# Kernel tuning notes

Measured on AMD Instinct MI355X. Metric: run time of the kernel, lower is better.

Reference implementation:

```python
import jax, jax.numpy as jnp
import numpy as np

N_NODES = 50000
N_EDGES = 800000
N_REL = 8
DIM = 256


def setup_inputs() -> dict:
    key = jax.random.key(0)
    ks = jax.random.split(key, 6)
    x = jax.random.normal(ks[0], (N_NODES, DIM), dtype=jnp.float32)
    # xavier-uniform-ish scale for [R, in, out] weights
    limit = float(np.sqrt(6.0 / (DIM + DIM)))
    W0 = jax.random.uniform(ks[1], (N_REL, DIM, DIM), dtype=jnp.float32, minval=-limit, maxval=limit)
    W1 = jax.random.uniform(ks[2], (N_REL, DIM, DIM), dtype=jnp.float32, minval=-limit, maxval=limit)
    b0 = jnp.zeros((DIM,), dtype=jnp.float32)
    b1 = jnp.zeros((DIM,), dtype=jnp.float32)
    edge_index = jax.random.randint(ks[3], (2, N_EDGES), 0, N_NODES, dtype=jnp.int64)
    edge_type = jax.random.randint(ks[4], (N_EDGES,), 0, N_REL, dtype=jnp.int64)
    return {"x": x, "W0": W0, "b0": b0, "W1": W1, "b1": b1,
            "edge_index": edge_index, "edge_type": edge_type}


def _rgcn_layer(x, W, b, src, dst, edge_type, num_nodes):
    # grouped GEMM over all relations: [R, N, out]
    xt = jnp.einsum('ni,rio->rno', x, W)
    # per-edge message = relu(x[src] @ W[edge_type] + b)  -> [E, out]
    msg = jax.nn.relu(xt[edge_type, src] + b)
    # scatter-add into destination nodes
    return jax.ops.segment_sum(msg, dst, num_segments=num_nodes)


def reference(x, W0, b0, W1, b1, edge_index, edge_type):
    src, dst = edge_index[0], edge_index[1]
    h = _rgcn_layer(x, W0, b0, src, dst, edge_type, x.shape[0])
    h = _rgcn_layer(h, W1, b1, src, dst, edge_type, x.shape[0])
    return h
```

## Files before the change

kernel.cpp:

```cpp
#include <hip/hip_runtime.h>

#define DIM 256
#define N_REL 8
#define NBLK 256
#define NBH 256

typedef __attribute__((ext_vector_type(8))) short short8_t;
typedef __attribute__((ext_vector_type(4))) float float4_t;

__device__ inline unsigned short f2bf(float f) {
    unsigned u = __float_as_uint(f);
    u += 0x7FFFu + ((u >> 16) & 1u);
    return (unsigned short)(u >> 16);
}
__device__ inline float bf2f(unsigned short h) {
    return __uint_as_float(((unsigned)h) << 16);
}

__global__ __launch_bounds__(256) void prep_mega(
    const float* __restrict__ x, unsigned short* __restrict__ xb, int n4,
    const float* __restrict__ W0, unsigned short* __restrict__ Wt0,
    const float* __restrict__ W1, unsigned short* __restrict__ Wt1,
    int nCast, int nW)
{
    __shared__ float tile[32][33];
    const int b = blockIdx.x;
    const int t = threadIdx.x;
    if (b < nCast) {
        const int i = b * 256 + t;
        if (i < n4) {
            const float4 v = ((const float4*)x)[i];
            ushort4 o;
            o.x = f2bf(v.x); o.y = f2bf(v.y); o.z = f2bf(v.z); o.w = f2bf(v.w);
            ((ushort4*)xb)[i] = o;
        }
    } else {
        const int wi = b - nCast;
        const float* W = (wi < nW) ? W0 : W1;
        unsigned short* Wt = (wi < nW) ? Wt0 : Wt1;
        const int bb = (wi < nW) ? wi : wi - nW;
        const int rel = bb >> 6;
        const int bx = bb & 7, by = (bb >> 3) & 7;
        const int i0 = bx * 32, o0 = by * 32;
        const int tx = t & 31, ty = t >> 5;
        const float* Wr = W + (size_t)rel * DIM * DIM;
        unsigned short* Wtr = Wt + (size_t)rel * DIM * DIM;
#pragma unroll
        for (int j = 0; j < 4; j++)
            tile[ty + 8 * j][tx] = Wr[(size_t)(i0 + ty + 8 * j) * DIM + o0 + tx];
        __syncthreads();
#pragma unroll
        for (int j = 0; j < 4; j++)
            Wtr[(size_t)(o0 + ty + 8 * j) * DIM + i0 + tx] =
                f2bf(tile[tx][ty + 8 * j]);
    }
}

__global__ __launch_bounds__(256) void build_keys_hist(
    const int* __restrict__ src, const int* __restrict__ dst,
    const int* __restrict__ et, int E,
    unsigned long long* __restrict__ e0, int* __restrict__ hist)
{
    __shared__ int lh[NBH];
    const int t = threadIdx.x, b = blockIdx.x;
    lh[t] = 0;
    __syncthreads();
    const int chunk = (E + NBLK - 1) / NBLK;
    const int lo = b * chunk, hi = min(lo + chunk, E);
    for (int i = lo + t; i < hi; i += 256) {
        const unsigned d = (unsigned)dst[i];
        e0[i] = ((unsigned long long)d << 32) |
                ((unsigned)((et[i] << 16) | src[i]));
        atomicAdd(&lh[d >> 8], 1);
    }
    __syncthreads();
    hist[t * NBLK + b] = lh[t];
}

__global__ __launch_bounds__(256) void scan_g_blocksums(
    const int* __restrict__ a, int n, int* __restrict__ bsum)
{
    __shared__ int red[256];
    const int t = threadIdx.x;
    const int base = blockIdx.x * 1024 + t * 4;
    int s = 0;
#pragma unroll
    for (int j = 0; j < 4; j++) {
        const int i = base + j;
        if (i < n) s += a[i];
    }
    red[t] = s;
    __syncthreads();
#pragma unroll
    for (int off = 128; off > 0; off >>= 1) {
        if (t < off) red[t] += red[t + off];
        __syncthreads();
    }
    if (t == 0) bsum[blockIdx.x] = red[0];
}

__global__ __launch_bounds__(256) void scan_g_write(
    const int* __restrict__ a, int n, const int* __restrict__ bsum, int nb,
    int* __restrict__ outArr, int* __restrict__ totalSlot)
{
    __shared__ int sb[64];
    __shared__ int sh[256];
    const int t = threadIdx.x;
    if (t < 64) sb[t] = (t < nb) ? bsum[t] : 0;
    __syncthreads();
    for (int off = 1; off < 64; off <<= 1) {
        int v = 0;
        if (t < 64) v = sb[t] + ((t >= off) ? sb[t - off] : 0);
        __syncthreads();
        if (t < 64) sb[t] = v;
        __syncthreads();
    }
    const int run0 = (blockIdx.x == 0) ? 0 : sb[blockIdx.x - 1];
    const int total = sb[nb - 1];

    const int base = blockIdx.x * 1024 + t * 4;
    int v[4];
#pragma unroll
    for (int j = 0; j < 4; j++) {
        const int i = base + j;
        v[j] = (i < n) ? a[i] : 0;
    }
    sh[t] = v[0] + v[1] + v[2] + v[3];
    __syncthreads();
    for (int off = 1; off < 256; off <<= 1) {
        const int add = (t >= off) ? sh[t - off] : 0;
        __syncthreads();
        sh[t] += add;
        __syncthreads();
    }
    int run = run0 + ((t == 0) ? 0 : sh[t - 1]);
#pragma unroll
    for (int j = 0; j < 4; j++) {
        const int i = base + j;
        if (i < n) outArr[i] = run;
        run += v[j];
    }
    if (totalSlot && (int)blockIdx.x == nb - 1 && t == 255) *totalSlot = total;
}

__global__ __launch_bounds__(256) void scatter_pass1(
    const unsigned long long* __restrict__ e0, int E,
    const int* __restrict__ histx, unsigned long long* __restrict__ e1)
{
    __shared__ int lbase[NBH];
    __shared__ int lrun[NBH];
    const int t = threadIdx.x, b = blockIdx.x;
    lbase[t] = histx[t * NBLK + b];
    lrun[t] = 0;
    __syncthreads();
    const int chunk = (E + NBLK - 1) / NBLK;
    const int lo = b * chunk, hi = min(lo + chunk, E);
    for (int i = lo + t; i < hi; i += 256) {
        const unsigned long long v = e0[i];
        const int bin = (int)(v >> 40) & 0xFF;
        const int pos = lbase[bin] + atomicAdd(&lrun[bin], 1);
        e1[pos] = v;
    }
}

__global__ __launch_bounds__(256) void bucket_sort(
    const unsigned long long* __restrict__ e1, int E,
    const int* __restrict__ histx,
    unsigned* __restrict__ ep, int* __restrict__ cnt)
{
    __shared__ int lh[256], lincl[256], lexcl[256], lrun[256];
    const int t = threadIdx.x;
    const int h = blockIdx.x;
    const int start = histx[h * NBLK];
    const int end = (h == NBH - 1) ? E : histx[(h + 1) * NBLK];
    if (end <= start) return;
    lh[t] = 0;
    __syncthreads();
    for (int i = start + t; i < end; i += 256)
        atomicAdd(&lh[(int)(e1[i] >> 32) & 0xFF], 1);
    __syncthreads();
    const int v = lh[t];
    lincl[t] = v;
    __syncthreads();
    for (int off = 1; off < 256; off <<= 1) {
        const int add = (t >= off) ? lincl[t - off] : 0;
        __syncthreads();
        lincl[t] += add;
        __syncthreads();
    }
    lexcl[t] = lincl[t] - v;
    lrun[t] = 0;
    if (v > 0) cnt[(h << 8) | t] = v;
    __syncthreads();
    for (int i = start + t; i < end; i += 256) {
        const unsigned long long x = e1[i];
        const int low = (int)(x >> 32) & 0xFF;
        const int pos = lexcl[low] + atomicAdd(&lrun[low], 1);
        ep[start + pos] = (unsigned)(x & 0xFFFFFFFFu);
    }
}

__global__ __launch_bounds__(256) void gemm_mfma_bias_relu(
    const unsigned short* __restrict__ Xb,
    const unsigned short* __restrict__ Wtb,
    const float* __restrict__ bias,
    unsigned short* __restrict__ Yall, int M, int Rtiles)
{
    __shared__ __align__(16) short smem[16384];

    const unsigned L = blockIdx.x;
    const int xcd = L & 7;
    const unsigned g = L >> 3;
    const int combo = g & 15;
    const int rt = (int)((g >> 4) << 3) | xcd;
    if (rt >= Rtiles) return;
    const int m0 = rt * 128;
    const int n0 = (combo & 1) * 128;
    const int rel = combo >> 1;

    const unsigned short* Wt = Wtb + (size_t)rel * DIM * DIM;
    unsigned short* Y = Yall + (size_t)rel * M * DIM;

    const int t = threadIdx.x;
    const int lane = t & 63;
    const int w = t >> 6;
    const int wr = w & 1, wc = w >> 1;
    const int r = lane & 15, q = lane >> 4;

    const int sl = lane & 3;
    const int rsub = lane >> 2;
    const unsigned short* gA[2];
    const unsigned short* gB[2];
#pragma unroll
    for (int h = 0; h < 2; h++) {
        const int row = h * 64 + w * 16 + rsub;
        const int gseg = sl ^ ((row >> 1) & 3);
        gA[h] = Xb + (size_t)(m0 + row) * DIM + gseg * 8;
        gB[h] = Wt + (size_t)(n0 + row) * DIM + gseg * 8;
    }

    const int swz = (q ^ ((r >> 1) & 3)) * 8;
    int offA[4], offB[4];
#pragma unroll
    for (int mi = 0; mi < 4; mi++)
        offA[mi] = (wr * 64 + mi * 16 + r) * 32 + swz;
#pragma unroll
    for (int ni = 0; ni < 4; ni++)
        offB[ni] = (wc * 64 + ni * 16 + r) * 32 + swz;

    float4_t acc[4][4];
#pragma unroll
    for (int i = 0; i < 4; i++)
#pragma unroll
        for (int j = 0; j < 4; j++) {
            float4_t z = {0.f, 0.f, 0.f, 0.f};
            acc[i][j] = z;
        }

#define STAGE(ks, bsel)                                                         \
    {                                                                           \
        const int k0_ = (ks) * 32;                                              \
        short* Ad_ = smem + ((bsel) ? 8192 : 0);                                \
        short* Bd_ = Ad_ + 4096;                                                \
        _Pragma("unroll")                                                       \
        for (int h = 0; h < 2; h++) {                                           \
            __builtin_amdgcn_global_load_lds(                                   \
                (const __attribute__((address_space(1))) unsigned int*)(gA[h] + k0_), \
                (__attribute__((address_space(3))) unsigned int*)(Ad_ + h * 2048 + w * 512), \
                16, 0, 0);                                                      \
            __builtin_amdgcn_global_load_lds(                                   \
                (const __attribute__((address_space(1))) unsigned int*)(gB[h] + k0_), \
                (__attribute__((address_space(3))) unsigned int*)(Bd_ + h * 2048 + w * 512), \
                16, 0, 0);                                                      \
        }                                                                       \
    }

    STAGE(0, 0);
#pragma unroll 1
    for (int ks = 0; ks < 8; ks++) {
        const int cur = ks & 1;
        if (ks < 7) {
            STAGE(ks + 1, cur ^ 1);
            asm volatile("s_waitcnt vmcnt(4)" ::: "memory");
        } else {
            asm volatile("s_waitcnt vmcnt(0)" ::: "memory");
        }
        asm volatile("s_barrier" ::: "memory");

        const short* As_b = smem + (cur ? 8192 : 0);
        const short* Bs_b = As_b + 4096;
        short8_t af[4], bf[4];
#pragma unroll
        for (int mi = 0; mi < 4; mi++)
            af[mi] = *(const short8_t*)&As_b[offA[mi]];
#pragma unroll
        for (int ni = 0; ni < 4; ni++)
            bf[ni] = *(const short8_t*)&Bs_b[offB[ni]];
#pragma unroll
        for (int mi = 0; mi < 4; mi++)
#pragma unroll
            for (int ni = 0; ni < 4; ni++)
                acc[mi][ni] = __builtin_amdgcn_mfma_f32_16x16x32_bf16(
                    af[mi], bf[ni], acc[mi][ni], 0, 0, 0);
        asm volatile("s_barrier" ::: "memory");
    }
#undef STAGE

    short* St = smem;

    float bv[4];
#pragma unroll
    for (int ni = 0; ni < 4; ni++)
        bv[ni] = bias[n0 + wc * 64 + ni * 16 + r];

#pragma unroll
    for (int mp = 0; mp < 2; mp++) {
#pragma unroll
        for (int s = 0; s < 2; s++) {
#pragma unroll
            for (int ni = 0; ni < 4; ni++) {
#pragma unroll
                for (int e = 0; e < 4; e++) {
                    const int rl = s * 32 + wr * 16 + q * 4 + e;
                    const int col = wc * 64 + ni * 16 + r;
                    St[rl * 136 + col] =
                        f2bf(fmaxf(acc[mp * 2 + s][ni][e] + bv[ni], 0.f));
                }
            }
        }
        __syncthreads();
#pragma unroll
        for (int j = 0; j < 4; j++) {
            const int id = t + 256 * j;
            const int rl2 = id >> 4;
            const int ch = id & 15;
            const int s = rl2 >> 5;
            const int rl = rl2 & 31;
            const int grow = m0 + (rl >> 4) * 64 + (mp * 2 + s) * 16 + (rl & 15);
            const short8_t v = *(const short8_t*)&St[rl2 * 136 + ch * 8];
            if (grow < M)
                *(short8_t*)&Y[(size_t)grow * DIM + n0 + ch * 8] = v;
        }
        if (mp == 0) __syncthreads();
    }
}

template <typename OT>
__global__ __launch_bounds__(256) void aggregate2x(
    const unsigned short* __restrict__ yall,
    const unsigned* __restrict__ ep, const int* __restrict__ rowptr,
    OT* __restrict__ out, int M)
{
    const int lane = threadIdx.x & 63;
    const int half = lane >> 5;
    const int cl = lane & 31;
    const int wv = (blockIdx.x * blockDim.x + threadIdx.x) >> 6;
    const int nw = (gridDim.x * blockDim.x) >> 6;
    const size_t plane = (size_t)M * DIM;
    const int npair = (M + 1) >> 1;

    for (int pr = wv; pr < npair; pr += nw) {
        const int d = 2 * pr + half;
        const bool live = (d < M);
        double acc[8];
#pragma unroll
        for (int j = 0; j < 8; j++) acc[j] = 0.0;

        int beg = 0, end = 0;
        if (live) { beg = rowptr[d]; end = rowptr[d + 1]; }

        for (int c0 = beg; c0 < end; c0 += 32) {
            const int n = min(32, end - c0);
            const unsigned myep = (c0 + cl < end) ? ep[c0 + cl] : 0u;
            for (int i = 0; i < n; i += 4) {
                short8_t u[4];
#pragma unroll
                for (int j = 0; j < 4; j++) {
                    const unsigned p = __shfl(myep, half * 32 + ((i + j) & 31));
                    u[j] = *(const short8_t*)(
                        yall + (size_t)(p >> 16) * plane +
                        (size_t)(p & 0xFFFFu) * DIM + cl * 8);
                }
#pragma unroll
                for (int j = 0; j < 4; j++) {
                    if (i + j < n) {
#pragma unroll
                        for (int k = 0; k < 8; k++)
                            acc[k] += (double)bf2f((unsigned short)u[j][k]);
                    }
                }
            }
        }
        if (live) {
            OT* dp = out + (size_t)d * DIM + cl * 8;
            if (sizeof(OT) == 4) {
                *(float4*)((float*)dp) = make_float4(
                    (float)acc[0], (float)acc[1], (float)acc[2], (float)acc[3]);
                *(float4*)((float*)dp + 4) = make_float4(
                    (float)acc[4], (float)acc[5], (float)acc[6], (float)acc[7]);
            } else {
                short8_t v;
#pragma unroll
                for (int j = 0; j < 8; j++) v[j] = (short)f2bf((float)acc[j]);
                *(short8_t*)((unsigned short*)dp) = v;
            }
        }
    }
}

__global__ __launch_bounds__(256) void gemm_bias_relu_f32(
    const float* __restrict__ A, const float* __restrict__ B,
    const float* __restrict__ bias, float* __restrict__ Y, int M)
{
    __shared__ float Asf[16][132];
    __shared__ float Bsf[16][128];
    const int t = threadIdx.x;
    const int tx = t & 15, ty = t >> 4;
    const int row0 = blockIdx.x * 128, col0 = blockIdx.y * 128;
    float acc[8][8];
#pragma unroll
    for (int i = 0; i < 8; i++)
#pragma unroll
        for (int j = 0; j < 8; j++) acc[i][j] = 0.f;
    const int arow = t >> 2, akseg = (t & 3) * 4;
    const int bk0 = t >> 5, bcol = (t & 31) * 4;
    for (int k0 = 0; k0 < DIM; k0 += 16) {
#pragma unroll
        for (int h = 0; h < 2; h++) {
            const int row = row0 + arow + h * 64;
            float4 av = (row < M) ? *(const float4*)(A + (size_t)row * DIM + k0 + akseg)
                                  : make_float4(0, 0, 0, 0);
            Asf[akseg + 0][arow + h * 64] = av.x;
            Asf[akseg + 1][arow + h * 64] = av.y;
            Asf[akseg + 2][arow + h * 64] = av.z;
            Asf[akseg + 3][arow + h * 64] = av.w;
        }
#pragma unroll
        for (int h = 0; h < 2; h++) {
            const int krow = bk0 + h * 8;
            *(float4*)&Bsf[krow][bcol] =
                *(const float4*)(B + (size_t)(k0 + krow) * DIM + col0 + bcol);
        }
        __syncthreads();
#pragma unroll
        for (int k = 0; k < 16; k++) {
            float a[8], b[8];
            *(float4*)&a[0] = *(const float4*)&Asf[k][ty * 4];
            *(float4*)&a[4] = *(const float4*)&Asf[k][64 + ty * 4];
            *(float4*)&b[0] = *(const float4*)&Bsf[k][tx * 4];
            *(float4*)&b[4] = *(const float4*)&Bsf[k][64 + tx * 4];
#pragma unroll
            for (int i = 0; i < 8; i++)
#pragma unroll
                for (int j = 0; j < 8; j++) acc[i][j] = fmaf(a[i], b[j], acc[i][j]);
        }
        __syncthreads();
    }
#pragma unroll
    for (int im = 0; im < 2; im++)
#pragma unroll
        for (int i = 0; i < 4; i++) {
            const int row = row0 + im * 64 + ty * 4 + i;
            if (row >= M) continue;
#pragma unroll
            for (int jm = 0; jm < 2; jm++) {
                const int col = col0 + jm * 64 + tx * 4;
                const float4 bb = *(const float4*)(bias + col);
                float4 o;
                o.x = fmaxf(acc[im * 4 + i][jm * 4 + 0] + bb.x, 0.f);
                o.y = fmaxf(acc[im * 4 + i][jm * 4 + 1] + bb.y, 0.f);
                o.z = fmaxf(acc[im * 4 + i][jm * 4 + 2] + bb.z, 0.f);
                o.w = fmaxf(acc[im * 4 + i][jm * 4 + 3] + bb.w, 0.f);
                *(float4*)(Y + (size_t)row * DIM + col) = o;
            }
        }
}

__global__ __launch_bounds__(256) void scatter_rel(
    const float* __restrict__ y, const int* __restrict__ src,
    const int* __restrict__ dst, const int* __restrict__ et,
    int rel, float* __restrict__ out, int n_edges)
{
    const int lane = threadIdx.x & 63;
    const int wave = (blockIdx.x * blockDim.x + threadIdx.x) >> 6;
    const int nwaves = (gridDim.x * blockDim.x) >> 6;
    for (int e = wave; e < n_edges; e += nwaves) {
        if (et[e] != rel) continue;
        const float4 v = *(const float4*)(y + (size_t)src[e] * DIM + lane * 4);
        float* o = out + (size_t)dst[e] * DIM + lane * 4;
        atomicAdd(o + 0, v.x);
        atomicAdd(o + 1, v.y);
        atomicAdd(o + 2, v.z);
        atomicAdd(o + 3, v.w);
    }
}

static inline size_t align16(size_t x) { return (x + 15) & ~(size_t)15; }

extern "C" void kernel_launch(void* const* d_in, const int* in_sizes, int n_in,
                              void* d_out, int out_size, void* d_ws, size_t ws_size,
                              hipStream_t stream)
{
    const float* x  = (const float*)d_in[0];
    const float* W0 = (const float*)d_in[1];
    const float* b0 = (const float*)d_in[2];
    const float* W1 = (const float*)d_in[3];
    const float* b1 = (const float*)d_in[4];
    const int* eidx = (const int*)d_in[5];
    const int* etyp = (const int*)d_in[6];

    const int M = in_sizes[0] / DIM;
    const int E = in_sizes[6];
    const int* src = eidx;
    const int* dst = eidx + E;
    float* out = (float*)d_out;

    const size_t plane = (size_t)M * DIM;
    const size_t wbytes = (size_t)N_REL * DIM * DIM * 2;
    const size_t yall_bytes = (size_t)N_REL * plane * 2;

    const size_t need = align16(plane * 2)
                      + align16(plane * 2)
                      + 2 * align16(wbytes)
                      + align16((size_t)(M + 1) * 4)
                      + align16((size_t)M * 4)
                      + align16((size_t)256 * 4)
                      + align16((size_t)NBH * NBLK * 4)
                      + align16((size_t)E * 4)
                      + align16(yall_bytes);

    if (M < 65536 && ws_size >= need && yall_bytes >= 2 * (size_t)E * 8) {
        char* ws = (char*)d_ws;
        size_t off = 0;
        unsigned short* h1b  = (unsigned short*)(ws + off); off = align16(off + plane * 2);
        unsigned short* xb   = (unsigned short*)(ws + off); off = align16(off + plane * 2);
        unsigned short* Wt0b = (unsigned short*)(ws + off); off = align16(off + wbytes);
        unsigned short* Wt1b = (unsigned short*)(ws + off); off = align16(off + wbytes);
        int* rowptr = (int*)(ws + off); off = align16(off + (size_t)(M + 1) * 4);
        int* cnt    = (int*)(ws + off); off = align16(off + (size_t)M * 4);
        int* bsum   = (int*)(ws + off); off = align16(off + (size_t)256 * 4);
        int* hist   = (int*)(ws + off); off = align16(off + (size_t)NBH * NBLK * 4);
        unsigned* ep = (unsigned*)(ws + off); off = align16(off + (size_t)E * 4);
        unsigned short* yall = (unsigned short*)(ws + off);
        unsigned long long* e64a = (unsigned long long*)yall;
        unsigned long long* e64b = e64a + E;

        const int n4 = (int)(plane / 4);
        const int nCast = (n4 + 255) / 256;
        const int nW = 512;
        prep_mega<<<nCast + 2 * nW, 256, 0, stream>>>(
            x, xb, n4, W0, Wt0b, W1, Wt1b, nCast, nW);

        hipMemsetAsync(cnt, 0, (size_t)M * 4, stream);
        build_keys_hist<<<NBLK, 256, 0, stream>>>(src, dst, etyp, E, e64a, hist);
        const int nhist = NBH * NBLK;
        const int nbh = (nhist + 1023) / 1024;
        scan_g_blocksums<<<nbh, 256, 0, stream>>>(hist, nhist, bsum);
        scan_g_write<<<nbh, 256, 0, stream>>>(hist, nhist, bsum, nbh, hist, (int*)nullptr);
        scatter_pass1<<<NBLK, 256, 0, stream>>>(e64a, E, hist, e64b);
        bucket_sort<<<NBH, 256, 0, stream>>>(e64b, E, hist, ep, cnt);
        const int nb = (M + 1023) / 1024;
        scan_g_blocksums<<<nb, 256, 0, stream>>>(cnt, M, bsum);
        scan_g_write<<<nb, 256, 0, stream>>>(cnt, M, bsum, nb, rowptr, &rowptr[M]);

        const int Rtiles = (M + 127) / 128;
        const int octets = (Rtiles + 7) / 8;
        const int ggrid = octets * 16 * 8;
        const int npair = (M + 1) / 2;
        const int agrid = (npair * 64 + 255) / 256;

        gemm_mfma_bias_relu<<<ggrid, 256, 0, stream>>>(xb, Wt0b, b0, yall, M, Rtiles);
        aggregate2x<unsigned short><<<agrid, 256, 0, stream>>>(yall, ep, rowptr, h1b, M);
        gemm_mfma_bias_relu<<<ggrid, 256, 0, stream>>>(h1b, Wt1b, b1, yall, M, Rtiles);
        aggregate2x<float><<<agrid, 256, 0, stream>>>(yall, ep, rowptr, out, M);
    } else {
        float* h1 = (float*)d_ws;
        float* y  = (float*)d_ws + plane;
        const dim3 gblk(256), ggrid2((M + 127) / 128, DIM / 128);
        hipMemsetAsync(h1, 0, plane * 4, stream);
        for (int r = 0; r < N_REL; r++) {
            gemm_bias_relu_f32<<<ggrid2, gblk, 0, stream>>>(
                x, W0 + (size_t)r * DIM * DIM, b0, y, M);
            scatter_rel<<<1024, 256, 0, stream>>>(y, src, dst, etyp, r, h1, E);
        }
        hipMemsetAsync(out, 0, plane * 4, stream);
        for (int r = 0; r < N_REL; r++) {
            gemm_bias_relu_f32<<<ggrid2, gblk, 0, stream>>>(
                h1, W1 + (size_t)r * DIM * DIM, b1, y, M);
            scatter_rel<<<1024, 256, 0, stream>>>(y, src, dst, etyp, r, out, E);
        }
    }
}
```

Before: 469.3 us.

## Split relations into two groups of four to halve the per-relation GEMM output buffer

Edges are now sorted by relation group (4 relations each) as well as destination, producing two CSR structures. Each layer runs two GEMM+aggregate passes over four relations at a time, keeping partial sums in an fp32 accumulator buffer. The intent is to shrink the bf16 transformed-feature buffer from 8 to 4 planes so the aggregation gathers hit a smaller working set that fits better in cache. The cost is extra kernel launches, an extra fp32 accumulator read/write per node, and a larger sort histogram.

```diff
diff --git a/kernel.cpp b/kernel.cpp
--- a/kernel.cpp
+++ b/kernel.cpp
@@ -3,7 +3,7 @@
 #define DIM 256
 #define N_REL 8
 #define NBLK 256
-#define NBH 256
+#define NBINS 512
 
 typedef __attribute__((ext_vector_type(8))) short short8_t;
 typedef __attribute__((ext_vector_type(4))) float float4_t;
@@ -61,20 +61,23 @@
     const int* __restrict__ et, int E,
     unsigned long long* __restrict__ e0, int* __restrict__ hist)
 {
-    __shared__ int lh[NBH];
+    __shared__ int lh[NBINS];
     const int t = threadIdx.x, b = blockIdx.x;
-    lh[t] = 0;
+    lh[t] = 0; lh[t + 256] = 0;
     __syncthreads();
     const int chunk = (E + NBLK - 1) / NBLK;
     const int lo = b * chunk, hi = min(lo + chunk, E);
     for (int i = lo + t; i < hi; i += 256) {
         const unsigned d = (unsigned)dst[i];
-        e0[i] = ((unsigned long long)d << 32) |
-                ((unsigned)((et[i] << 16) | src[i]));
-        atomicAdd(&lh[d >> 8], 1);
+        const unsigned e = (unsigned)et[i];
+        const unsigned g = e >> 2;
+        e0[i] = ((unsigned long long)((g << 16) | d) << 32) |
+                ((e << 16) | (unsigned)src[i]);
+        atomicAdd(&lh[(g << 8) | (d >> 8)], 1);
     }
     __syncthreads();
     hist[t * NBLK + b] = lh[t];
+    hist[(t + 256) * NBLK + b] = lh[t + 256];
 }
 
 __global__ __launch_bounds__(256) void scan_g_blocksums(
@@ -103,16 +106,15 @@
     const int* __restrict__ a, int n, const int* __restrict__ bsum, int nb,
     int* __restrict__ outArr, int* __restrict__ totalSlot)
 {
-    __shared__ int sb[64];
+    __shared__ int sb[256];
     __shared__ int sh[256];
     const int t = threadIdx.x;
-    if (t < 64) sb[t] = (t < nb) ? bsum[t] : 0;
-    __syncthreads();
-    for (int off = 1; off < 64; off <<= 1) {
-        int v = 0;
-        if (t < 64) v = sb[t] + ((t >= off) ? sb[t - off] : 0);
-        __syncthreads();
-        if (t < 64) sb[t] = v;
+    sb[t] = (t < nb) ? bsum[t] : 0;
+    __syncthreads();
+    for (int off = 1; off < 256; off <<= 1) {
+        const int v = sb[t] + ((t >= off) ? sb[t - off] : 0);
+        __syncthreads();
+        sb[t] = v;
         __syncthreads();
     }
     const int run0 = (blockIdx.x == 0) ? 0 : sb[blockIdx.x - 1];
@@ -147,17 +149,18 @@
     const unsigned long long* __restrict__ e0, int E,
     const int* __restrict__ histx, unsigned long long* __restrict__ e1)
 {
-    __shared__ int lbase[NBH];
-    __shared__ int lrun[NBH];
+    __shared__ int lbase[NBINS];
+    __shared__ int lrun[NBINS];
     const int t = threadIdx.x, b = blockIdx.x;
     lbase[t] = histx[t * NBLK + b];
-    lrun[t] = 0;
+    lbase[t + 256] = histx[(t + 256) * NBLK + b];
+    lrun[t] = 0; lrun[t + 256] = 0;
     __syncthreads();
     const int chunk = (E + NBLK - 1) / NBLK;
     const int lo = b * chunk, hi = min(lo + chunk, E);
     for (int i = lo + t; i < hi; i += 256) {
         const unsigned long long v = e0[i];
-        const int bin = (int)(v >> 40) & 0xFF;
+        const int bin = (int)(v >> 40) & 0x1FF;
         const int pos = lbase[bin] + atomicAdd(&lrun[bin], 1);
         e1[pos] = v;
     }
@@ -166,13 +169,13 @@
 __global__ __launch_bounds__(256) void bucket_sort(
     const unsigned long long* __restrict__ e1, int E,
     const int* __restrict__ histx,
-    unsigned* __restrict__ ep, int* __restrict__ cnt)
+    unsigned* __restrict__ ep, int* __restrict__ cnt2, int M)
 {
     __shared__ int lh[256], lincl[256], lexcl[256], lrun[256];
     const int t = threadIdx.x;
     const int h = blockIdx.x;
     const int start = histx[h * NBLK];
-    const int end = (h == NBH - 1) ? E : histx[(h + 1) * NBLK];
+    const int end = (h == NBINS - 1) ? E : histx[(h + 1) * NBLK];
     if (end <= start) return;
     lh[t] = 0;
     __syncthreads();
@@ -190,7 +193,11 @@
     }
     lexcl[t] = lincl[t] - v;
     lrun[t] = 0;
-    if (v > 0) cnt[(h << 8) | t] = v;
+    if (v > 0) {
+        const int g = h >> 8;
+        const int d = ((h & 0xFF) << 8) | t;
+        cnt2[g * M + d] = v;
+    }
     __syncthreads();
     for (int i = start + t; i < end; i += 256) {
         const unsigned long long x = e1[i];
@@ -204,22 +211,22 @@
     const unsigned short* __restrict__ Xb,
     const unsigned short* __restrict__ Wtb,
     const float* __restrict__ bias,
-    unsigned short* __restrict__ Yall, int M, int Rtiles)
+    unsigned short* __restrict__ Yg, int M, int Rtiles)
 {
     __shared__ __align__(16) short smem[16384];
 
     const unsigned L = blockIdx.x;
     const int xcd = L & 7;
-    const unsigned g = L >> 3;
-    const int combo = g & 15;
-    const int rt = (int)((g >> 4) << 3) | xcd;
+    const unsigned gg = L >> 3;
+    const int combo = gg & 7;
+    const int rt = (int)((gg >> 3) << 3) | xcd;
     if (rt >= Rtiles) return;
     const int m0 = rt * 128;
     const int n0 = (combo & 1) * 128;
     const int rel = combo >> 1;
 
     const unsigned short* Wt = Wtb + (size_t)rel * DIM * DIM;
-    unsigned short* Y = Yall + (size_t)rel * M * DIM;
+    unsigned short* Y = Yg + (size_t)rel * M * DIM;
 
     const int t = threadIdx.x;
     const int lane = t & 63;
@@ -345,11 +352,11 @@
     }
 }
 
-template <typename OT>
-__global__ __launch_bounds__(256) void aggregate2x(
-    const unsigned short* __restrict__ yall,
+template <int PHASE, typename OT>
+__global__ __launch_bounds__(256) void aggregate_half(
+    const unsigned short* __restrict__ yg,
     const unsigned* __restrict__ ep, const int* __restrict__ rowptr,
-    OT* __restrict__ out, int M)
+    float* __restrict__ acc, OT* __restrict__ out, int M)
 {
     const int lane = threadIdx.x & 63;
     const int half = lane >> 5;
@@ -362,9 +369,9 @@
     for (int pr = wv; pr < npair; pr += nw) {
         const int d = 2 * pr + half;
         const bool live = (d < M);
-        double acc[8];
-#pragma unroll
-        for (int j = 0; j < 8; j++) acc[j] = 0.0;
+        double s[8];
+#pragma unroll
+        for (int j = 0; j < 8; j++) s[j] = 0.0;
 
         int beg = 0, end = 0;
         if (live) { beg = rowptr[d]; end = rowptr[d + 1]; }
@@ -378,7 +385,7 @@
                 for (int j = 0; j < 4; j++) {
                     const unsigned p = __shfl(myep, half * 32 + ((i + j) & 31));
                     u[j] = *(const short8_t*)(
-                        yall + (size_t)(p >> 16) * plane +
+                        yg + (size_t)((p >> 16) & 3) * plane +
                         (size_t)(p & 0xFFFFu) * DIM + cl * 8);
                 }
 #pragma unroll
@@ -386,23 +393,36 @@
                     if (i + j < n) {
 #pragma unroll
                         for (int k = 0; k < 8; k++)
-                            acc[k] += (double)bf2f((unsigned short)u[j][k]);
+                            s[k] += (double)bf2f((unsigned short)u[j][k]);
                     }
                 }
             }
         }
         if (live) {
-            OT* dp = out + (size_t)d * DIM + cl * 8;
-            if (sizeof(OT) == 4) {
-                *(float4*)((float*)dp) = make_float4(
-                    (float)acc[0], (float)acc[1], (float)acc[2], (float)acc[3]);
-                *(float4*)((float*)dp + 4) = make_float4(
-                    (float)acc[4], (float)acc[5], (float)acc[6], (float)acc[7]);
+            float* ar = acc + (size_t)d * DIM + cl * 8;
+            if (PHASE == 0) {
+                *(float4*)ar = make_float4(
+                    (float)s[0], (float)s[1], (float)s[2], (float)s[3]);
+                *((float4*)ar + 1) = make_float4(
+                    (float)s[4], (float)s[5], (float)s[6], (float)s[7]);
             } else {
-                short8_t v;
-#pragma unroll
-                for (int j = 0; j < 8; j++) v[j] = (short)f2bf((float)acc[j]);
-                *(short8_t*)((unsigned short*)dp) = v;
+                const float4 a0 = *(const float4*)ar;
+                const float4 a1 = *((const float4*)ar + 1);
+                float tot[8];
+                tot[0] = a0.x + (float)s[0]; tot[1] = a0.y + (float)s[1];
+                tot[2] = a0.z + (float)s[2]; tot[3] = a0.w + (float)s[3];
+                tot[4] = a1.x + (float)s[4]; tot[5] = a1.y + (float)s[5];
+                tot[6] = a1.z + (float)s[6]; tot[7] = a1.w + (float)s[7];
+                OT* dp = out + (size_t)d * DIM + cl * 8;
+                if (sizeof(OT) == 4) {
+                    *(float4*)((float*)dp) = make_float4(tot[0], tot[1], tot[2], tot[3]);
+                    *(float4*)((float*)dp + 4) = make_float4(tot[4], tot[5], tot[6], tot[7]);
+                } else {
+                    short8_t v;
+#pragma unroll
+                    for (int j = 0; j < 8; j++) v[j] = (short)f2bf(tot[j]);
+                    *(short8_t*)((unsigned short*)dp) = v;
+                }
             }
         }
     }
@@ -517,32 +537,34 @@
 
     const size_t plane = (size_t)M * DIM;
     const size_t wbytes = (size_t)N_REL * DIM * DIM * 2;
-    const size_t yall_bytes = (size_t)N_REL * plane * 2;
+    const size_t ybuf_bytes = (size_t)4 * plane * 2;
 
     const size_t need = align16(plane * 2)
                       + align16(plane * 2)
                       + 2 * align16(wbytes)
-                      + align16((size_t)(M + 1) * 4)
-                      + align16((size_t)M * 4)
+                      + align16((size_t)(2 * M + 1) * 4)
+                      + align16((size_t)2 * M * 4)
                       + align16((size_t)256 * 4)
-                      + align16((size_t)NBH * NBLK * 4)
+                      + align16((size_t)NBINS * NBLK * 4)
                       + align16((size_t)E * 4)
-                      + align16(yall_bytes);
-
-    if (M < 65536 && ws_size >= need && yall_bytes >= 2 * (size_t)E * 8) {
+                      + align16(plane * 4)
+                      + align16(ybuf_bytes);
+
+    if (M < 65536 && ws_size >= need && ybuf_bytes >= 2 * (size_t)E * 8) {
         char* ws = (char*)d_ws;
         size_t off = 0;
         unsigned short* h1b  = (unsigned short*)(ws + off); off = align16(off + plane * 2);
         unsigned short* xb   = (unsigned short*)(ws + off); off = align16(off + plane * 2);
         unsigned short* Wt0b = (unsigned short*)(ws + off); off = align16(off + wbytes);
         unsigned short* Wt1b = (unsigned short*)(ws + off); off = align16(off + wbytes);
-        int* rowptr = (int*)(ws + off); off = align16(off + (size_t)(M + 1) * 4);
-        int* cnt    = (int*)(ws + off); off = align16(off + (size_t)M * 4);
-        int* bsum   = (int*)(ws + off); off = align16(off + (size_t)256 * 4);
-        int* hist   = (int*)(ws + off); off = align16(off + (size_t)NBH * NBLK * 4);
+        int* rowptr2 = (int*)(ws + off); off = align16(off + (size_t)(2 * M + 1) * 4);
+        int* cnt2    = (int*)(ws + off); off = align16(off + (size_t)2 * M * 4);
+        int* bsum    = (int*)(ws + off); off = align16(off + (size_t)256 * 4);
+        int* hist    = (int*)(ws + off); off = align16(off + (size_t)NBINS * NBLK * 4);
         unsigned* ep = (unsigned*)(ws + off); off = align16(off + (size_t)E * 4);
-        unsigned short* yall = (unsigned short*)(ws + off);
-        unsigned long long* e64a = (unsigned long long*)yall;
+        float* acc   = (float*)(ws + off); off = align16(off + plane * 4);
+        unsigned short* ybuf = (unsigned short*)(ws + off);
+        unsigned long long* e64a = (unsigned long long*)ybuf;
         unsigned long long* e64b = e64a + E;
 
         const int n4 = (int)(plane / 4);
@@ -551,28 +573,38 @@
         prep_mega<<<nCast + 2 * nW, 256, 0, stream>>>(
             x, xb, n4, W0, Wt0b, W1, Wt1b, nCast, nW);
 
-        hipMemsetAsync(cnt, 0, (size_t)M * 4, stream);
+        hipMemsetAsync(cnt2, 0, (size_t)2 * M * 4, stream);
         build_keys_hist<<<NBLK, 256, 0, stream>>>(src, dst, etyp, E, e64a, hist);
-        const int nhist = NBH * NBLK;
+        const int nhist = NBINS * NBLK;
         const int nbh = (nhist + 1023) / 1024;
         scan_g_blocksums<<<nbh, 256, 0, stream>>>(hist, nhist, bsum);
         scan_g_write<<<nbh, 256, 0, stream>>>(hist, nhist, bsum, nbh, hist, (int*)nullptr);
         scatter_pass1<<<NBLK, 256, 0, stream>>>(e64a, E, hist, e64b);
-        bucket_sort<<<NBH, 256, 0, stream>>>(e64b, E, hist, ep, cnt);
-        const int nb = (M + 1023) / 1024;
-        scan_g_blocksums<<<nb, 256, 0, stream>>>(cnt, M, bsum);
-        scan_g_write<<<nb, 256, 0, stream>>>(cnt, M, bsum, nb, rowptr, &rowptr[M]);
+        bucket_sort<<<NBINS, 256, 0, stream>>>(e64b, E, hist, ep, cnt2, M);
+        const int n2m = 2 * M;
+        const int nb2 = (n2m + 1023) / 1024;
+        scan_g_blocksums<<<nb2, 256, 0, stream>>>(cnt2, n2m, bsum);
+        scan_g_write<<<nb2, 256, 0, stream>>>(cnt2, n2m, bsum, nb2, rowptr2, &rowptr2[n2m]);
 
         const int Rtiles = (M + 127) / 128;
         const int octets = (Rtiles + 7) / 8;
-        const int ggrid = octets * 16 * 8;
+        const int ggrid = octets * 8 * 8;
         const int npair = (M + 1) / 2;
         const int agrid = (npair * 64 + 255) / 256;
-
-        gemm_mfma_bias_relu<<<ggrid, 256, 0, stream>>>(xb, Wt0b, b0, yall, M, Rtiles);
-        aggregate2x<unsigned short><<<agrid, 256, 0, stream>>>(yall, ep, rowptr, h1b, M);
-        gemm_mfma_bias_relu<<<ggrid, 256, 0, stream>>>(h1b, Wt1b, b1, yall, M, Rtiles);
-        aggregate2x<float><<<agrid, 256, 0, stream>>>(yall, ep, rowptr, out, M);
+        const size_t wgrp = (size_t)4 * DIM * DIM;
+
+        gemm_mfma_bias_relu<<<ggrid, 256, 0, stream>>>(xb, Wt0b, b0, ybuf, M, Rtiles);
+        aggregate_half<0, unsigned short><<<agrid, 256, 0, stream>>>(
+            ybuf, ep, rowptr2, acc, h1b, M);
+        gemm_mfma_bias_relu<<<ggrid, 256, 0, stream>>>(xb, Wt0b + wgrp, b0, ybuf, M, Rtiles);
+        aggregate_half<1, unsigned short><<<agrid, 256, 0, stream>>>(
+            ybuf, ep, rowptr2 + M, acc, h1b, M);
+        gemm_mfma_bias_relu<<<ggrid, 256, 0, stream>>>(h1b, Wt1b, b1, ybuf, M, Rtiles);
+        aggregate_half<0, float><<<agrid, 256, 0, stream>>>(
+            ybuf, ep, rowptr2, acc, out, M);
+        gemm_mfma_bias_relu<<<ggrid, 256, 0, stream>>>(h1b, Wt1b + wgrp, b1, ybuf, M, Rtiles);
+        aggregate_half<1, float><<<agrid, 256, 0, stream>>>(
+            ybuf, ep, rowptr2 + M, acc, out, M);
     } else {
         float* h1 = (float*)d_ws;
         float* y  = (float*)d_ws + plane;
```

Result: slower. 514.7 us (+9.7%).

## Fuse preprocessing and CSR construction into one cooperative kernel with grid syncs

Applied to the files above, without the earlier changes.

Replaces the chain of small kernels (cast/transpose, key build, histogram scans, two-level scatter sort, rowptr scans) and a memset with a single cooperative kernel of 256 blocks that separates the phases with grid-wide syncs. This removes several launch gaps and the memset. In exchange the cast and transpose work now runs on only 256 blocks with grid-stride loops, which lowers parallelism for the bandwidth-bound conversion, and each grid sync carries its own cost.

```diff
diff --git a/kernel.cpp b/kernel.cpp
--- a/kernel.cpp
+++ b/kernel.cpp
@@ -1,9 +1,8 @@
 #include <hip/hip_runtime.h>
+#include <hip/hip_cooperative_groups.h>
 
 #define DIM 256
 #define N_REL 8
-#define NBLK 256
-#define NBH 256
 
 typedef __attribute__((ext_vector_type(8))) short short8_t;
 typedef __attribute__((ext_vector_type(4))) float float4_t;
@@ -17,186 +16,179 @@
     return __uint_as_float(((unsigned)h) << 16);
 }
 
-__global__ __launch_bounds__(256) void prep_mega(
+__global__ __launch_bounds__(256) void fused_prep_csr(
     const float* __restrict__ x, unsigned short* __restrict__ xb, int n4,
     const float* __restrict__ W0, unsigned short* __restrict__ Wt0,
     const float* __restrict__ W1, unsigned short* __restrict__ Wt1,
-    int nCast, int nW)
+    const int* __restrict__ src, const int* __restrict__ dstp,
+    const int* __restrict__ et, int E,
+    int* __restrict__ hist, int* __restrict__ bsum,
+    unsigned long long* __restrict__ e0, unsigned long long* __restrict__ e1,
+    unsigned* __restrict__ ep, int* __restrict__ cnt,
+    int* __restrict__ rowptr, int M)
 {
-    __shared__ float tile[32][33];
-    const int b = blockIdx.x;
-    const int t = threadIdx.x;
-    if (b < nCast) {
-        const int i = b * 256 + t;
-        if (i < n4) {
-            const float4 v = ((const float4*)x)[i];
-            ushort4 o;
-            o.x = f2bf(v.x); o.y = f2bf(v.y); o.z = f2bf(v.z); o.w = f2bf(v.w);
-            ((ushort4*)xb)[i] = o;
-        }
-    } else {
-        const int wi = b - nCast;
-        const float* W = (wi < nW) ? W0 : W1;
-        unsigned short* Wt = (wi < nW) ? Wt0 : Wt1;
-        const int bb = (wi < nW) ? wi : wi - nW;
-        const int rel = bb >> 6;
-        const int bx = bb & 7, by = (bb >> 3) & 7;
-        const int i0 = bx * 32, o0 = by * 32;
+    __shared__ __align__(16) int sarena[1088];
+    const int t = threadIdx.x, b = blockIdx.x;
+
+    for (int i = b * 256 + t; i < n4; i += 65536) {
+        const float4 v = ((const float4*)x)[i];
+        ushort4 o;
+        o.x = f2bf(v.x); o.y = f2bf(v.y); o.z = f2bf(v.z); o.w = f2bf(v.w);
+        ((ushort4*)xb)[i] = o;
+    }
+    {
+        float (*tile)[33] = (float(*)[33])sarena;
         const int tx = t & 31, ty = t >> 5;
-        const float* Wr = W + (size_t)rel * DIM * DIM;
-        unsigned short* Wtr = Wt + (size_t)rel * DIM * DIM;
-#pragma unroll
-        for (int j = 0; j < 4; j++)
-            tile[ty + 8 * j][tx] = Wr[(size_t)(i0 + ty + 8 * j) * DIM + o0 + tx];
-        __syncthreads();
-#pragma unroll
-        for (int j = 0; j < 4; j++)
-            Wtr[(size_t)(o0 + ty + 8 * j) * DIM + i0 + tx] =
-                f2bf(tile[tx][ty + 8 * j]);
-    }
-}
-
-__global__ __launch_bounds__(256) void build_keys_hist(
-    const int* __restrict__ src, const int* __restrict__ dst,
-    const int* __restrict__ et, int E,
-    unsigned long long* __restrict__ e0, int* __restrict__ hist)
-{
-    __shared__ int lh[NBH];
-    const int t = threadIdx.x, b = blockIdx.x;
-    lh[t] = 0;
-    __syncthreads();
-    const int chunk = (E + NBLK - 1) / NBLK;
-    const int lo = b * chunk, hi = min(lo + chunk, E);
-    for (int i = lo + t; i < hi; i += 256) {
-        const unsigned d = (unsigned)dst[i];
-        e0[i] = ((unsigned long long)d << 32) |
-                ((unsigned)((et[i] << 16) | src[i]));
-        atomicAdd(&lh[d >> 8], 1);
-    }
-    __syncthreads();
-    hist[t * NBLK + b] = lh[t];
-}
-
-__global__ __launch_bounds__(256) void scan_g_blocksums(
-    const int* __restrict__ a, int n, int* __restrict__ bsum)
-{
-    __shared__ int red[256];
-    const int t = threadIdx.x;
-    const int base = blockIdx.x * 1024 + t * 4;
-    int s = 0;
-#pragma unroll
-    for (int j = 0; j < 4; j++) {
-        const int i = base + j;
-        if (i < n) s += a[i];
-    }
-    red[t] = s;
-    __syncthreads();
-#pragma unroll
-    for (int off = 128; off > 0; off >>= 1) {
-        if (t < off) red[t] += red[t + off];
-        __syncthreads();
-    }
-    if (t == 0) bsum[blockIdx.x] = red[0];
-}
-
-__global__ __launch_bounds__(256) void scan_g_write(
-    const int* __restrict__ a, int n, const int* __restrict__ bsum, int nb,
-    int* __restrict__ outArr, int* __restrict__ totalSlot)
-{
-    __shared__ int sb[64];
-    __shared__ int sh[256];
-    const int t = threadIdx.x;
-    if (t < 64) sb[t] = (t < nb) ? bsum[t] : 0;
-    __syncthreads();
-    for (int off = 1; off < 64; off <<= 1) {
-        int v = 0;
-        if (t < 64) v = sb[t] + ((t >= off) ? sb[t - off] : 0);
-        __syncthreads();
-        if (t < 64) sb[t] = v;
-        __syncthreads();
-    }
-    const int run0 = (blockIdx.x == 0) ? 0 : sb[blockIdx.x - 1];
-    const int total = sb[nb - 1];
-
-    const int base = blockIdx.x * 1024 + t * 4;
-    int v[4];
-#pragma unroll
-    for (int j = 0; j < 4; j++) {
-        const int i = base + j;
-        v[j] = (i < n) ? a[i] : 0;
-    }
-    sh[t] = v[0] + v[1] + v[2] + v[3];
-    __syncthreads();
-    for (int off = 1; off < 256; off <<= 1) {
-        const int add = (t >= off) ? sh[t - off] : 0;
-        __syncthreads();
-        sh[t] += add;
-        __syncthreads();
-    }
-    int run = run0 + ((t == 0) ? 0 : sh[t - 1]);
-#pragma unroll
-    for (int j = 0; j < 4; j++) {
-        const int i = base + j;
-        if (i < n) outArr[i] = run;
-        run += v[j];
-    }
-    if (totalSlot && (int)blockIdx.x == nb - 1 && t == 255) *totalSlot = total;
-}
-
-__global__ __launch_bounds__(256) void scatter_pass1(
-    const unsigned long long* __restrict__ e0, int E,
-    const int* __restrict__ histx, unsigned long long* __restrict__ e1)
-{
-    __shared__ int lbase[NBH];
-    __shared__ int lrun[NBH];
-    const int t = threadIdx.x, b = blockIdx.x;
-    lbase[t] = histx[t * NBLK + b];
-    lrun[t] = 0;
-    __syncthreads();
-    const int chunk = (E + NBLK - 1) / NBLK;
-    const int lo = b * chunk, hi = min(lo + chunk, E);
-    for (int i = lo + t; i < hi; i += 256) {
-        const unsigned long long v = e0[i];
-        const int bin = (int)(v >> 40) & 0xFF;
-        const int pos = lbase[bin] + atomicAdd(&lrun[bin], 1);
-        e1[pos] = v;
-    }
-}
-
-__global__ __launch_bounds__(256) void bucket_sort(
-    const unsigned long long* __restrict__ e1, int E,
-    const int* __restrict__ histx,
-    unsigned* __restrict__ ep, int* __restrict__ cnt)
-{
-    __shared__ int lh[256], lincl[256], lexcl[256], lrun[256];
-    const int t = threadIdx.x;
-    const int h = blockIdx.x;
-    const int start = histx[h * NBLK];
-    const int end = (h == NBH - 1) ? E : histx[(h + 1) * NBLK];
-    if (end <= start) return;
-    lh[t] = 0;
-    __syncthreads();
-    for (int i = start + t; i < end; i += 256)
-        atomicAdd(&lh[(int)(e1[i] >> 32) & 0xFF], 1);
-    __syncthreads();
-    const int v = lh[t];
-    lincl[t] = v;
-    __syncthreads();
-    for (int off = 1; off < 256; off <<= 1) {
-        const int add = (t >= off) ? lincl[t - off] : 0;
-        __syncthreads();
-        lincl[t] += add;
-        __syncthreads();
-    }
-    lexcl[t] = lincl[t] - v;
-    lrun[t] = 0;
-    if (v > 0) cnt[(h << 8) | t] = v;
-    __syncthreads();
-    for (int i = start + t; i < end; i += 256) {
-        const unsigned long long x = e1[i];
-        const int low = (int)(x >> 32) & 0xFF;
-        const int pos = lexcl[low] + atomicAdd(&lrun[low], 1);
-        ep[start + pos] = (unsigned)(x & 0xFFFFFFFFu);
+        for (int job = b; job < 1024; job += 256) {
+            const float* W = (job < 512) ? W0 : W1;
+            unsigned short* Wt = (job < 512) ? Wt0 : Wt1;
+            const int bb = job & 511;
+            const int rel = bb >> 6;
+            const int bx = bb & 7, by = (bb >> 3) & 7;
+            const int i0 = bx * 32, o0 = by * 32;
+            const float* Wr = W + (size_t)rel * DIM * DIM;
+            unsigned short* Wtr = Wt + (size_t)rel * DIM * DIM;
+            __syncthreads();
+#pragma unroll
+            for (int j = 0; j < 4; j++)
+                tile[ty + 8 * j][tx] = Wr[(size_t)(i0 + ty + 8 * j) * DIM + o0 + tx];
+            __syncthreads();
+#pragma unroll
+            for (int j = 0; j < 4; j++)
+                Wtr[(size_t)(o0 + ty + 8 * j) * DIM + i0 + tx] =
+                    f2bf(tile[tx][ty + 8 * j]);
+        }
+    }
+    {
+        int* lh = sarena;
+        __syncthreads();
+        lh[t] = 0;
+        __syncthreads();
+        const int chunk = (E + 255) >> 8;
+        const int lo = b * chunk, hi = min(lo + chunk, E);
+        for (int i = lo + t; i < hi; i += 256) {
+            const unsigned d = (unsigned)dstp[i];
+            e0[i] = ((unsigned long long)d << 32) |
+                    ((unsigned)((et[i] << 16) | src[i]));
+            atomicAdd(&lh[d >> 8], 1);
+        }
+        __syncthreads();
+        hist[t * 256 + b] = lh[t];
+    }
+    cooperative_groups::this_grid().sync();
+    int myexcl;
+    {
+        int* sh = sarena;
+        const int v = hist[b * 256 + t];
+        __syncthreads();
+        sh[t] = v;
+        __syncthreads();
+        for (int off = 1; off < 256; off <<= 1) {
+            const int add = (t >= off) ? sh[t - off] : 0;
+            __syncthreads();
+            sh[t] += add;
+            __syncthreads();
+        }
+        if (t == 255) bsum[b] = sh[255];
+        myexcl = sh[t] - v;
+    }
+    cooperative_groups::this_grid().sync();
+    {
+        int* sb = sarena;
+        __syncthreads();
+        sb[t] = bsum[t];
+        __syncthreads();
+        for (int off = 1; off < 256; off <<= 1) {
+            const int add = (t >= off) ? sb[t - off] : 0;
+            __syncthreads();
+            sb[t] += add;
+            __syncthreads();
+        }
+        const int pre = (b == 0) ? 0 : sb[b - 1];
+        hist[b * 256 + t] = pre + myexcl;
+    }
+    cooperative_groups::this_grid().sync();
+    {
+        int* lbase = sarena;
+        int* lrun = sarena + 256;
+        __syncthreads();
+        lbase[t] = hist[t * 256 + b];
+        lrun[t] = 0;
+        __syncthreads();
+        const int chunk = (E + 255) >> 8;
+        const int lo = b * chunk, hi = min(lo + chunk, E);
+        for (int i = lo + t; i < hi; i += 256) {
+            const unsigned long long v = e0[i];
+            const int bin = (int)(v >> 40) & 0xFF;
+            const int pos = lbase[bin] + atomicAdd(&lrun[bin], 1);
+            e1[pos] = v;
+        }
+    }
+    cooperative_groups::this_grid().sync();
+    {
+        int* lh = sarena;
+        int* lincl = sarena + 256;
+        int* lexcl = sarena + 512;
+        int* lrun = sarena + 768;
+        const int start = hist[b * 256];
+        const int end = (b == 255) ? E : hist[(b + 1) * 256];
+        __syncthreads();
+        lh[t] = 0;
+        __syncthreads();
+        for (int i = start + t; i < end; i += 256)
+            atomicAdd(&lh[(int)(e1[i] >> 32) & 0xFF], 1);
+        __syncthreads();
+        const int v = lh[t];
+        lincl[t] = v;
+        __syncthreads();
+        for (int off = 1; off < 256; off <<= 1) {
+            const int add = (t >= off) ? lincl[t - off] : 0;
+            __syncthreads();
+            lincl[t] += add;
+            __syncthreads();
+        }
+        lexcl[t] = lincl[t] - v;
+        lrun[t] = 0;
+        const int d = (b << 8) | t;
+        if (d < M) cnt[d] = v;
+        __syncthreads();
+        for (int i = start + t; i < end; i += 256) {
+            const unsigned long long xk = e1[i];
+            const int low = (int)(xk >> 32) & 0xFF;
+            const int pos = lexcl[low] + atomicAdd(&lrun[low], 1);
+            ep[start + pos] = (unsigned)(xk & 0xFFFFFFFFu);
+        }
+    }
+    cooperative_groups::this_grid().sync();
+    {
+        int* s5 = sarena;
+        const int c2 = (M + 255) >> 8;
+        const int idx = b * c2 + t;
+        const int v5 = (t < c2 && idx < M) ? cnt[idx] : 0;
+        __syncthreads();
+        s5[t] = v5;
+        __syncthreads();
+        for (int off = 1; off < 256; off <<= 1) {
+            const int add = (t >= off) ? s5[t - off] : 0;
+            __syncthreads();
+            s5[t] += add;
+            __syncthreads();
+        }
+        if (t == 255) bsum[b] = s5[255];
+        const int excl5 = s5[t] - v5;
+        cooperative_groups::this_grid().sync();
+        __syncthreads();
+        s5[t] = bsum[t];
+        __syncthreads();
+        for (int off = 1; off < 256; off <<= 1) {
+            const int add = (t >= off) ? s5[t - off] : 0;
+            __syncthreads();
+            s5[t] += add;
+            __syncthreads();
+        }
+        const int pre5 = (b == 0) ? 0 : s5[b - 1];
+        if (t < c2 && idx < M) rowptr[idx] = pre5 + excl5;
+        if (b == 255 && t == 0) rowptr[M] = E;
     }
 }
 
@@ -444,15 +436,15 @@
         __syncthreads();
 #pragma unroll
         for (int k = 0; k < 16; k++) {
-            float a[8], b[8];
+            float a[8], bvv[8];
             *(float4*)&a[0] = *(const float4*)&Asf[k][ty * 4];
             *(float4*)&a[4] = *(const float4*)&Asf[k][64 + ty * 4];
-            *(float4*)&b[0] = *(const float4*)&Bsf[k][tx * 4];
-            *(float4*)&b[4] = *(const float4*)&Bsf[k][64 + tx * 4];
+            *(float4*)&bvv[0] = *(const float4*)&Bsf[k][tx * 4];
+            *(float4*)&bvv[4] = *(const float4*)&Bsf[k][64 + tx * 4];
 #pragma unroll
             for (int i = 0; i < 8; i++)
 #pragma unroll
-                for (int j = 0; j < 8; j++) acc[i][j] = fmaf(a[i], b[j], acc[i][j]);
+                for (int j = 0; j < 8; j++) acc[i][j] = fmaf(a[i], bvv[j], acc[i][j]);
         }
         __syncthreads();
     }
@@ -525,7 +517,7 @@
                       + align16((size_t)(M + 1) * 4)
                       + align16((size_t)M * 4)
                       + align16((size_t)256 * 4)
-                      + align16((size_t)NBH * NBLK * 4)
+                      + align16((size_t)256 * 256 * 4)
                       + align16((size_t)E * 4)
                       + align16(yall_bytes);
 
@@ -539,29 +531,22 @@
         int* rowptr = (int*)(ws + off); off = align16(off + (size_t)(M + 1) * 4);
         int* cnt    = (int*)(ws + off); off = align16(off + (size_t)M * 4);
         int* bsum   = (int*)(ws + off); off = align16(off + (size_t)256 * 4);
-        int* hist   = (int*)(ws + off); off = align16(off + (size_t)NBH * NBLK * 4);
+        int* hist   = (int*)(ws + off); off = align16(off + (size_t)256 * 256 * 4);
         unsigned* ep = (unsigned*)(ws + off); off = align16(off + (size_t)E * 4);
         unsigned short* yall = (unsigned short*)(ws + off);
         unsigned long long* e64a = (unsigned long long*)yall;
         unsigned long long* e64b = e64a + E;
 
-        const int n4 = (int)(plane / 4);
-        const int nCast = (n4 + 255) / 256;
-        const int nW = 512;
-        prep_mega<<<nCast + 2 * nW, 256, 0, stream>>>(
-            x, xb, n4, W0, Wt0b, W1, Wt1b, nCast, nW);
-
-        hipMemsetAsync(cnt, 0, (size_t)M * 4, stream);
-        build_keys_hist<<<NBLK, 256, 0, stream>>>(src, dst, etyp, E, e64a, hist);
-        const int nhist = NBH * NBLK;
-        const int nbh = (nhist + 1023) / 1024;
-        scan_g_blocksums<<<nbh, 256, 0, stream>>>(hist, nhist, bsum);
-        scan_g_write<<<nbh, 256, 0, stream>>>(hist, nhist, bsum, nbh, hist, (int*)nullptr);
-        scatter_pass1<<<NBLK, 256, 0, stream>>>(e64a, E, hist, e64b);
-        bucket_sort<<<NBH, 256, 0, stream>>>(e64b, E, hist, ep, cnt);
-        const int nb = (M + 1023) / 1024;
-        scan_g_blocksums<<<nb, 256, 0, stream>>>(cnt, M, bsum);
-        scan_g_write<<<nb, 256, 0, stream>>>(cnt, M, bsum, nb, rowptr, &rowptr[M]);
+        int n4 = (int)(plane / 4);
+        int Ei = E, Mi = M;
+        void* cargs[] = {
+            (void*)&x, (void*)&xb, (void*)&n4,
+            (void*)&W0, (void*)&Wt0b, (void*)&W1, (void*)&Wt1b,
+            (void*)&src, (void*)&dst, (void*)&etyp, (void*)&Ei,
+            (void*)&hist, (void*)&bsum, (void*)&e64a, (void*)&e64b,
+            (void*)&ep, (void*)&cnt, (void*)&rowptr, (void*)&Mi };
+        hipLaunchCooperativeKernel((const void*)fused_prep_csr,
+                                   dim3(256), dim3(256), cargs, 0, stream);
 
         const int Rtiles = (M + 127) / 128;
         const int octets = (Rtiles + 7) / 8;
```

Result: slower. 669.8 us (+42.7%).
